# Optimization experiments

Hardware: AMD Instinct MI355X
Metric: run time of the kernel (lower is better)

## Reference

```python
import jax, jax.numpy as jnp
import numpy as np
import math

EMBED_DIM = 1024
NUM_HEADS = 16
HEAD_DIM = EMBED_DIM // NUM_HEADS


def setup_inputs() -> dict:
    key = jax.random.key(0)
    ks = jax.random.split(key, 12)
    B, N = 2, 2048
    s = 1.0 / math.sqrt(EMBED_DIM)
    inp = {
        "query": jax.random.normal(ks[0], (B, N, EMBED_DIM), jnp.float32),
        "key": jax.random.normal(ks[1], (B, N, EMBED_DIM), jnp.float32),
        "value": jax.random.normal(ks[2], (B, N, EMBED_DIM), jnp.float32),
        "Wq": jax.random.normal(ks[3], (EMBED_DIM, EMBED_DIM), jnp.float32) * s,
        "bq": jnp.zeros((EMBED_DIM,), jnp.float32),
        "Wk": jax.random.normal(ks[4], (EMBED_DIM, EMBED_DIM), jnp.float32) * s,
        "bk": jnp.zeros((EMBED_DIM,), jnp.float32),
        "Wv": jax.random.normal(ks[5], (EMBED_DIM, EMBED_DIM), jnp.float32) * s,
        "bv": jnp.zeros((EMBED_DIM,), jnp.float32),
        "Wo": jax.random.normal(ks[6], (EMBED_DIM, EMBED_DIM), jnp.float32) * s,
        "bo": jnp.zeros((EMBED_DIM,), jnp.float32),
        "gate": jnp.zeros((NUM_HEADS,), jnp.float32),
    }
    return inp


def reference(query, key, value, Wq, bq, Wk, bk, Wv, bv, Wo, bo, gate):
    B, Nq, _ = query.shape
    Nk = key.shape[1]
    H, D = NUM_HEADS, HEAD_DIM
    # projections (Linear: x @ W.T + b); split heads -> [B, H, N, D]
    q = (query @ Wq.T + bq).reshape(B, Nq, H, D).transpose(0, 2, 1, 3)
    k = (key @ Wk.T + bk).reshape(B, Nk, H, D).transpose(0, 2, 1, 3)
    v = (value @ Wv.T + bv).reshape(B, Nk, H, D).transpose(0, 2, 1, 3)
    # scaled logits with per-head sigmoid gate folded into the scale
    scale = jax.nn.sigmoid(gate) / math.sqrt(D)  # [H]
    logits = jnp.einsum("bhqd,bhkd->bhqk", q, k) * scale[None, :, None, None]
    attn = jax.nn.softmax(logits, axis=-1)
    out = jnp.einsum("bhqk,bhkd->bhqd", attn, v)
    out = out.transpose(0, 2, 1, 3).reshape(B, Nq, H * D)
    return out @ Wo.T + bo
```

## Files before the change

kernel.cpp:

```cpp
#include <hip/hip_runtime.h>
#include <hip/hip_bf16.h>
#include <cstdint>


#define DEV __device__ __forceinline__
typedef __attribute__((ext_vector_type(8))) short bf16x8;
typedef __attribute__((ext_vector_type(4))) float f32x4;
typedef unsigned short u16;

DEV void async16(const void* g, void* l) {
  __builtin_amdgcn_global_load_lds(
      (const __attribute__((address_space(1))) unsigned int*)g,
      (__attribute__((address_space(3))) unsigned int*)l, 16, 0, 0);
}

DEV u16 bf16_rne(float f) {
  unsigned int u = __builtin_bit_cast(unsigned int, f);
  u += 0x7FFFu + ((u >> 16) & 1u);
  return (u16)(u >> 16);
}

DEV u16 cvt16(float x) {
  __hip_bfloat16 h = __float2bfloat16(x);
  return __builtin_bit_cast(u16, h);
}

DEV unsigned cvtpk(float lo, float hi) {
  unsigned r;
  asm("v_cvt_pk_bf16_f32 %0, %1, %2" : "=v"(r) : "v"(lo), "v"(hi));
  return r;
}

DEV uint4 cvt8(float4 a, float4 b) {
  uint4 v;
  v.x = cvtpk(a.x, a.y);
  v.y = cvtpk(a.z, a.w);
  v.z = cvtpk(b.x, b.y);
  v.w = cvtpk(b.z, b.w);
  return v;
}

__global__ __launch_bounds__(256, 3) void gemm_qkv(
    const float* __restrict__ Xq, const float* __restrict__ Xk, const float* __restrict__ Xv,
    const float* __restrict__ Wqf, const float* __restrict__ Wkf, const float* __restrict__ Wvf,
    const float* __restrict__ bq, const float* __restrict__ bkb, const float* __restrict__ bv,
    const float* __restrict__ gate,
    u16* __restrict__ QB, u16* __restrict__ KB, u16* __restrict__ VTB) {
  __shared__ __attribute__((aligned(16))) u16 As[2][128 * 32];
  __shared__ __attribute__((aligned(16))) u16 Bs[2][128 * 32];
  const int t = threadIdx.x, lane = t & 63, w = t >> 6;
  const int l15 = lane & 15, quad = lane >> 4;
  const int xcd = blockIdx.x & 7, idx = blockIdx.x >> 3;
  const int seg = idx >> 5, r5 = idx & 31;
  const int bm = (xcd << 2) + (r5 >> 3), bn = r5 & 7;
  const int m0 = bm << 7, n0 = bn << 7;
  const float* A = (seg == 0) ? Xq : (seg == 1) ? Xk : Xv;
  const float* W = (seg == 0) ? Wqf : (seg == 1) ? Wkf : Wvf;
  const int wm = (w >> 1) << 6, wn = (w & 1) << 6;
  const int r0 = t >> 2, cc0 = (t & 3) * 8;
  const float* gA0 = A + (long)(m0 + r0) * 1024 + cc0;
  const float* gA1 = gA0 + 64 * 1024;
  const float* gB0 = W + (long)(n0 + r0) * 1024 + cc0;
  const float* gB1 = gB0 + 64 * 1024;

  float4 ra0, ra1, ra2, ra3, rb0, rb1, rb2, rb3;
  auto LOADA = [&](int ko) {
    const float4* p0 = (const float4*)(gA0 + ko);
    const float4* p1 = (const float4*)(gA1 + ko);
    ra0 = p0[0]; ra1 = p0[1]; ra2 = p1[0]; ra3 = p1[1];
  };
  auto LOADB = [&](int ko) {
    const float4* p0 = (const float4*)(gB0 + ko);
    const float4* p1 = (const float4*)(gB1 + ko);
    rb0 = p0[0]; rb1 = p0[1]; rb2 = p1[0]; rb3 = p1[1];
  };
  auto WRITEA = [&](int nb) {
    *(uint4*)&As[nb][t * 8] = cvt8(ra0, ra1);
    *(uint4*)&As[nb][(t + 256) * 8] = cvt8(ra2, ra3);
  };
  auto WRITEB = [&](int nb) {
    *(uint4*)&Bs[nb][t * 8] = cvt8(rb0, rb1);
    *(uint4*)&Bs[nb][(t + 256) * 8] = cvt8(rb2, rb3);
  };

  LOADA(0); LOADB(0);
  WRITEA(0); WRITEB(0);
  LOADA(32); LOADB(32);

  f32x4 acc[4][4] = {};
  for (int k0 = 0; k0 < 1024; k0 += 32) {
    const int cur = (k0 >> 5) & 1;
    __syncthreads();
    if (k0 + 32 < 1024) {
      const int nb = cur ^ 1;
      WRITEA(nb); WRITEB(nb);
      if (k0 + 64 < 1024) { LOADA(k0 + 64); LOADB(k0 + 64); }
    }
    bf16x8 af[4], bfm[4];
#pragma unroll
    for (int i = 0; i < 4; i++)
      af[i] = *(const bf16x8*)&As[cur][(wm + i * 16 + l15) * 32 + quad * 8];
#pragma unroll
    for (int j = 0; j < 4; j++)
      bfm[j] = *(const bf16x8*)&Bs[cur][(wn + j * 16 + l15) * 32 + quad * 8];
#pragma unroll
    for (int i = 0; i < 4; i++)
#pragma unroll
      for (int j = 0; j < 4; j++)
        acc[i][j] = __builtin_amdgcn_mfma_f32_16x16x32_bf16(af[i], bfm[j], acc[i][j], 0, 0, 0);
  }

  if (seg == 2) {
#pragma unroll
    for (int i = 0; i < 4; i++) {
      int token = m0 + wm + i * 16 + quad * 4;
      int bb_ = token >> 11, n = token & 2047;
#pragma unroll
      for (int j = 0; j < 4; j++) {
        int col = n0 + wn + j * 16 + l15;
        float bb = bv[col];
        union { u16 us[4]; uint2 u2; } pk;
#pragma unroll
        for (int r = 0; r < 4; r++) pk.us[r] = bf16_rne(acc[i][j][r] + bb);
        *(uint2*)&VTB[(long)(bb_ * 1024 + col) * 2048 + n] = pk.u2;
      }
    }
  } else {
    const float* bias = seg ? bkb : bq;
    u16* C = seg ? KB : QB;
#pragma unroll
    for (int j = 0; j < 4; j++) {
      int col = n0 + wn + j * 16 + l15;
      float bb = bias[col];
      float scl = 1.f;
      if (seg == 0) {
        float g = gate[col >> 6];
        float sig = 1.f / (1.f + __builtin_amdgcn_exp2f(-g * 1.44269504f));
        scl = sig * 0.125f * 1.44269504f;
      }
#pragma unroll
      for (int i = 0; i < 4; i++) {
        int row = m0 + wm + i * 16 + quad * 4;
#pragma unroll
        for (int r = 0; r < 4; r++)
          C[(long)(row + r) * 1024 + col] = bf16_rne((acc[i][j][r] + bb) * scl);
      }
    }
  }
}

__global__ __launch_bounds__(256, 4) void gemm_out(
    const u16* __restrict__ A, const float* __restrict__ Wof,
    const float* __restrict__ bias, float* __restrict__ Cf) {
  __shared__ __attribute__((aligned(16))) u16 As[2][64 * 32];
  __shared__ __attribute__((aligned(16))) u16 Bs[2][64 * 32];
  const int t = threadIdx.x, lane = t & 63, w = t >> 6;
  const int l15 = lane & 15, quad = lane >> 4;
  const int xcd = blockIdx.x & 7, idx = blockIdx.x >> 3;
  const int bm = (xcd << 3) + (idx >> 4), bn = idx & 15;
  const int m0 = bm << 6, n0 = bn << 6;
  const int wm = (w >> 1) << 5, wn = (w & 1) << 5;
  const int r0 = t >> 2, cc0 = (t & 3) * 8;
  const u16* gA = A + (long)(m0 + r0) * 1024 + cc0;
  const float* gB = Wof + (long)(n0 + r0) * 1024 + cc0;

  float4 rb0, rb1;
  auto LOADB = [&](int ko) {
    const float4* p = (const float4*)(gB + ko);
    rb0 = p[0]; rb1 = p[1];
  };
  auto WRITEB = [&](int nb) {
    *(uint4*)&Bs[nb][t * 8] = cvt8(rb0, rb1);
  };

  async16(gA, &As[0][t * 8]);
  LOADB(0); WRITEB(0); LOADB(32);

  f32x4 acc[2][2] = {};
  for (int k0 = 0; k0 < 1024; k0 += 32) {
    const int cur = (k0 >> 5) & 1;
    __syncthreads();
    if (k0 + 32 < 1024) {
      const int kn = k0 + 32, nb = cur ^ 1;
      async16(gA + kn, &As[nb][t * 8]);
      WRITEB(nb);
      if (k0 + 64 < 1024) LOADB(k0 + 64);
    }
    bf16x8 af[2], bfm[2];
#pragma unroll
    for (int i = 0; i < 2; i++)
      af[i] = *(const bf16x8*)&As[cur][(wm + i * 16 + l15) * 32 + quad * 8];
#pragma unroll
    for (int j = 0; j < 2; j++)
      bfm[j] = *(const bf16x8*)&Bs[cur][(wn + j * 16 + l15) * 32 + quad * 8];
#pragma unroll
    for (int i = 0; i < 2; i++)
#pragma unroll
      for (int j = 0; j < 2; j++)
        acc[i][j] = __builtin_amdgcn_mfma_f32_16x16x32_bf16(af[i], bfm[j], acc[i][j], 0, 0, 0);
  }

#pragma unroll
  for (int j = 0; j < 2; j++) {
    int col = n0 + wn + j * 16 + l15;
    float bb = bias[col];
#pragma unroll
    for (int i = 0; i < 2; i++) {
      int row = m0 + wm + i * 16 + quad * 4;
#pragma unroll
      for (int r = 0; r < 4; r++)
        Cf[(long)(row + r) * 1024 + col] = acc[i][j][r] + bb;
    }
  }
}

__global__ __launch_bounds__(256, 4) void attn_kernel(
    const u16* __restrict__ Q, const u16* __restrict__ Kb,
    const u16* __restrict__ Vt, u16* __restrict__ Op0, u16* __restrict__ Op3,
    float* __restrict__ lp) {
  __shared__ __attribute__((aligned(16))) u16 Ks[2][32 * 64];
  __shared__ __attribute__((aligned(16))) u16 Vs[2][64 * 32];
  const int t = threadIdx.x, lane = t & 63, w = t >> 6;
  const int l15 = lane & 15, quad = lane >> 4;
  const int xcd = blockIdx.x & 7, rr = blockIdx.x >> 3;
  const int ksp = xcd >> 1, qt = ((xcd & 1) << 3) | rr;
  const int h = blockIdx.y, b = blockIdx.z;
  const int q0 = qt * 128, tok0 = b * 2048, key0 = ksp * 512;
  const u16* Kbase = Kb + (long)tok0 * 1024 + h * 64;
  const u16* Vbase = Vt + (long)(b * 1024 + h * 64) * 2048 + key0;

  bf16x8 aq[2][2];
#pragma unroll
  for (int i = 0; i < 2; i++) {
    long row = tok0 + q0 + w * 32 + i * 16 + l15;
#pragma unroll
    for (int ks = 0; ks < 2; ks++)
      aq[i][ks] = *(const bf16x8*)&Q[row * 1024 + h * 64 + ks * 32 + quad * 8];
  }

  const int rk = t >> 3, ck = t & 7;
  const int rv = t >> 2, cv = t & 3;
  const u16* kg = Kbase + (long)(key0 + rk) * 1024 + ((ck ^ ((rk >> 1) & 7)) * 8);
  const u16* vg = Vbase + (long)rv * 2048 + ((cv ^ ((rv >> 1) & 3)) * 8);
  u16* ksd = &Ks[0][t * 8];
  u16* vsd = &Vs[0][t * 8];

  auto STAGE = [&](int tk, int bu) {
    async16(kg + (long)tk * 32768, ksd + bu * 2048);
    async16(vg + tk * 32, vsd + bu * 2048);
  };

  STAGE(0, 0);

  float l_st[2] = {};
  f32x4 O[2][4] = {};

  for (int kt = 0; kt < 16; kt++) {
    const int cur = kt & 1;
    __syncthreads();
    if (kt + 1 < 16) STAGE(kt + 1, cur ^ 1);

    f32x4 s[2][2] = {};
    __builtin_amdgcn_s_setprio(1);
#pragma unroll
    for (int ks = 0; ks < 2; ks++) {
      bf16x8 bk_[2];
#pragma unroll
      for (int j = 0; j < 2; j++) {
        int rl = 2 * l15 + j;
        bk_[j] = *(const bf16x8*)&Ks[cur][rl * 64 + (((ks * 4 + quad) ^ (l15 & 7))) * 8];
      }
#pragma unroll
      for (int i = 0; i < 2; i++)
#pragma unroll
        for (int j = 0; j < 2; j++)
          s[i][j] = __builtin_amdgcn_mfma_f32_16x16x32_bf16(bk_[j], aq[i][ks], s[i][j], 0, 0, 0);
    }
    __builtin_amdgcn_s_setprio(0);

    bf16x8 ap[2];
#pragma unroll
    for (int i = 0; i < 2; i++) {
      union { unsigned uw[4]; bf16x8 v8; } pw;
#pragma unroll
      for (int r = 0; r < 4; r++) {
        float p0 = __builtin_amdgcn_exp2f(s[i][0][r]);
        float p1 = __builtin_amdgcn_exp2f(s[i][1][r]);
        l_st[i] += p0 + p1;
        pw.uw[r] = cvtpk(p0, p1);
      }
      ap[i] = pw.v8;
    }

    bf16x8 bv_[4];
#pragma unroll
    for (int dj = 0; dj < 4; dj++) {
      int rl = dj * 16 + l15;
      bv_[dj] = *(const bf16x8*)&Vs[cur][rl * 32 + ((quad ^ ((rl >> 1) & 3))) * 8];
    }
    __builtin_amdgcn_s_setprio(1);
#pragma unroll
    for (int i = 0; i < 2; i++)
#pragma unroll
      for (int dj = 0; dj < 4; dj++)
        O[i][dj] = __builtin_amdgcn_mfma_f32_16x16x32_bf16(ap[i], bv_[dj], O[i][dj], 0, 0, 0);
    __builtin_amdgcn_s_setprio(0);
  }

  u16* dst = (ksp == 3) ? Op3 : (Op0 + (long)ksp * 4194304);
#pragma unroll
  for (int i = 0; i < 2; i++) {
    float ls = l_st[i];
    ls += __shfl_xor(ls, 16); ls += __shfl_xor(ls, 32);
    if (quad == 0) {
      long qrow = tok0 + q0 + w * 32 + i * 16 + l15;
      lp[ksp * 65536 + (int)qrow * 16 + h] = ls;
    }
#pragma unroll
    for (int r = 0; r < 4; r++) {
      long row = tok0 + q0 + w * 32 + i * 16 + quad * 4 + r;
#pragma unroll
      for (int dj = 0; dj < 4; dj++)
        dst[row * 1024 + h * 64 + dj * 16 + l15] = cvt16(O[i][dj][r]);
    }
  }
}

__global__ __launch_bounds__(256) void merge_kernel(
    const u16* __restrict__ Op0, const u16* __restrict__ Op3,
    const float* __restrict__ lp, u16* __restrict__ AO) {
  int idx = blockIdx.x * 256 + threadIdx.x;
  int tok = idx >> 7, rem = idx & 127, h = rem >> 3;
  int li = tok * 16 + h;
  float inv = 1.f / (lp[li] + lp[65536 + li] + lp[131072 + li] + lp[196608 + li]);
  union U { uint4 v; u16 us[8]; };
  U a0, a1, a2, a3, uo;
  a0.v = ((const uint4*)Op0)[idx];
  a1.v = ((const uint4*)Op0)[idx + 524288];
  a2.v = ((const uint4*)Op0)[idx + 1048576];
  a3.v = ((const uint4*)Op3)[idx];
#pragma unroll
  for (int j = 0; j < 8; j++) {
    float f0 = __builtin_bit_cast(float, (unsigned)((unsigned)a0.us[j] << 16));
    float f1 = __builtin_bit_cast(float, (unsigned)((unsigned)a1.us[j] << 16));
    float f2 = __builtin_bit_cast(float, (unsigned)((unsigned)a2.us[j] << 16));
    float f3 = __builtin_bit_cast(float, (unsigned)((unsigned)a3.us[j] << 16));
    uo.us[j] = cvt16((f0 + f1 + f2 + f3) * inv);
  }
  ((uint4*)AO)[idx] = uo.v;
}

extern "C" void kernel_launch(void* const* d_in, const int* in_sizes, int n_in,
                              void* d_out, int out_size, void* d_ws, size_t ws_size,
                              hipStream_t stream) {
  const float* q  = (const float*)d_in[0];
  const float* k  = (const float*)d_in[1];
  const float* v  = (const float*)d_in[2];
  const float* Wq = (const float*)d_in[3];
  const float* bq = (const float*)d_in[4];
  const float* Wk = (const float*)d_in[5];
  const float* bk = (const float*)d_in[6];
  const float* Wv = (const float*)d_in[7];
  const float* bv = (const float*)d_in[8];
  const float* Wo = (const float*)d_in[9];
  const float* bo = (const float*)d_in[10];
  const float* gate = (const float*)d_in[11];
  float* out = (float*)d_out;
  char* ws = (char*)d_ws;

  const size_t MB = 1u << 20;
  u16* QB  = (u16*)(ws + 32 * MB);
  u16* KB  = (u16*)(ws + 40 * MB);
  u16* OPp  = (u16*)(ws + 8 * MB);
  u16* OPd3 = (u16*)((char*)d_out + 8 * MB);
  float* LP = (float*)(ws + 0 * MB);
  u16* AOB  = (u16*)(ws + 8 * MB);
  u16* VTB  = (u16*)d_out;

  gemm_qkv<<<768, 256, 0, stream>>>(q, k, v, Wq, Wk, Wv, bq, bk, bv, gate,
                                    QB, KB, VTB);
  attn_kernel<<<dim3(64, 16, 2), 256, 0, stream>>>(QB, KB, VTB, OPp, OPd3, LP);
  merge_kernel<<<2048, 256, 0, stream>>>(OPp, OPd3, LP, AOB);
  gemm_out<<<1024, 256, 0, stream>>>(AOB, Wo, bo, out);
}
```

Before: 230.5 us.

## Pre-cast QKV weights to bf16, halve key splits, fuse merge into output GEMM

Adds a pre-pass that casts Wq/Wk/Wv to bf16 so the QKV GEMM can stream the B operand straight into LDS with async loads instead of converting fp32 in registers. Attention now uses 2 key splits of 1024 keys instead of 4 of 512, launching half as many blocks, each doing twice as many key tiles. The separate merge kernel is removed: the output GEMM reads the two partial outputs and the row sums, combines and normalizes them while staging its A tile. This saves a launch and a full pass over intermediate data, at the cost of less attention parallelism, an extra cast kernel, and register-path loads in the output GEMM.

```diff
diff --git a/kernel.cpp b/kernel.cpp
--- a/kernel.cpp
+++ b/kernel.cpp
@@ -40,9 +40,25 @@
   return v;
 }
 
+DEV float bfu(u16 u) {
+  return __builtin_bit_cast(float, (unsigned)((unsigned)u << 16));
+}
+
+__global__ __launch_bounds__(256) void cast_w(
+    const float* __restrict__ Wq, const float* __restrict__ Wk,
+    const float* __restrict__ Wv, u16* __restrict__ WB) {
+  int idx = blockIdx.x * 256 + threadIdx.x;
+  const float* src; int i;
+  if      (idx < 131072) { src = Wq; i = idx; }
+  else if (idx < 262144) { src = Wk; i = idx - 131072; }
+  else                   { src = Wv; i = idx - 262144; }
+  const float4* p = (const float4*)src + (size_t)i * 2;
+  ((uint4*)WB)[idx] = cvt8(p[0], p[1]);
+}
+
 __global__ __launch_bounds__(256, 3) void gemm_qkv(
     const float* __restrict__ Xq, const float* __restrict__ Xk, const float* __restrict__ Xv,
-    const float* __restrict__ Wqf, const float* __restrict__ Wkf, const float* __restrict__ Wvf,
+    const u16* __restrict__ Wb,
     const float* __restrict__ bq, const float* __restrict__ bkb, const float* __restrict__ bv,
     const float* __restrict__ gate,
     u16* __restrict__ QB, u16* __restrict__ KB, u16* __restrict__ VTB) {
@@ -55,46 +71,39 @@
   const int bm = (xcd << 2) + (r5 >> 3), bn = r5 & 7;
   const int m0 = bm << 7, n0 = bn << 7;
   const float* A = (seg == 0) ? Xq : (seg == 1) ? Xk : Xv;
-  const float* W = (seg == 0) ? Wqf : (seg == 1) ? Wkf : Wvf;
+  const u16* W = Wb + (long)seg * 1048576;
   const int wm = (w >> 1) << 6, wn = (w & 1) << 6;
   const int r0 = t >> 2, cc0 = (t & 3) * 8;
   const float* gA0 = A + (long)(m0 + r0) * 1024 + cc0;
   const float* gA1 = gA0 + 64 * 1024;
-  const float* gB0 = W + (long)(n0 + r0) * 1024 + cc0;
-  const float* gB1 = gB0 + 64 * 1024;
-
-  float4 ra0, ra1, ra2, ra3, rb0, rb1, rb2, rb3;
+  const u16* gB0 = W + (long)(n0 + r0) * 1024 + cc0;
+  const u16* gB1 = gB0 + 64 * 1024;
+
+  float4 ra0, ra1, ra2, ra3;
   auto LOADA = [&](int ko) {
     const float4* p0 = (const float4*)(gA0 + ko);
     const float4* p1 = (const float4*)(gA1 + ko);
     ra0 = p0[0]; ra1 = p0[1]; ra2 = p1[0]; ra3 = p1[1];
   };
-  auto LOADB = [&](int ko) {
-    const float4* p0 = (const float4*)(gB0 + ko);
-    const float4* p1 = (const float4*)(gB1 + ko);
-    rb0 = p0[0]; rb1 = p0[1]; rb2 = p1[0]; rb3 = p1[1];
-  };
   auto WRITEA = [&](int nb) {
     *(uint4*)&As[nb][t * 8] = cvt8(ra0, ra1);
     *(uint4*)&As[nb][(t + 256) * 8] = cvt8(ra2, ra3);
   };
-  auto WRITEB = [&](int nb) {
-    *(uint4*)&Bs[nb][t * 8] = cvt8(rb0, rb1);
-    *(uint4*)&Bs[nb][(t + 256) * 8] = cvt8(rb2, rb3);
-  };
-
-  LOADA(0); LOADB(0);
-  WRITEA(0); WRITEB(0);
-  LOADA(32); LOADB(32);
+
+  LOADA(0);
+  async16(gB0, &Bs[0][t * 8]); async16(gB1, &Bs[0][(t + 256) * 8]);
+  WRITEA(0);
+  LOADA(32);
 
   f32x4 acc[4][4] = {};
   for (int k0 = 0; k0 < 1024; k0 += 32) {
     const int cur = (k0 >> 5) & 1;
     __syncthreads();
     if (k0 + 32 < 1024) {
-      const int nb = cur ^ 1;
-      WRITEA(nb); WRITEB(nb);
-      if (k0 + 64 < 1024) { LOADA(k0 + 64); LOADB(k0 + 64); }
+      const int kn = k0 + 32, nb = cur ^ 1;
+      WRITEA(nb);
+      async16(gB0 + kn, &Bs[nb][t * 8]); async16(gB1 + kn, &Bs[nb][(t + 256) * 8]);
+      if (k0 + 64 < 1024) LOADA(k0 + 64);
     }
     bf16x8 af[4], bfm[4];
 #pragma unroll
@@ -150,8 +159,9 @@
 }
 
 __global__ __launch_bounds__(256, 4) void gemm_out(
-    const u16* __restrict__ A, const float* __restrict__ Wof,
-    const float* __restrict__ bias, float* __restrict__ Cf) {
+    const u16* __restrict__ Op0, const float* __restrict__ lp,
+    const float* __restrict__ Wof, const float* __restrict__ bias,
+    float* __restrict__ Cf) {
   __shared__ __attribute__((aligned(16))) u16 As[2][64 * 32];
   __shared__ __attribute__((aligned(16))) u16 Bs[2][64 * 32];
   const int t = threadIdx.x, lane = t & 63, w = t >> 6;
@@ -161,10 +171,28 @@
   const int m0 = bm << 6, n0 = bn << 6;
   const int wm = (w >> 1) << 5, wn = (w & 1) << 5;
   const int r0 = t >> 2, cc0 = (t & 3) * 8;
-  const u16* gA = A + (long)(m0 + r0) * 1024 + cc0;
+  const uint4* gA0u = (const uint4*)Op0 + (((long)(m0 + r0) * 1024 + cc0) >> 3);
   const float* gB = Wof + (long)(n0 + r0) * 1024 + cc0;
 
+  uint4 au0, au1; float ainv;
   float4 rb0, rb1;
+  auto LOADA = [&](int ko) {
+    au0 = gA0u[ko >> 3];
+    au1 = gA0u[524288 + (ko >> 3)];
+    int li = (m0 + r0) * 16 + (ko >> 6);
+    ainv = 1.f / (lp[li] + lp[65536 + li]);
+  };
+  auto WRITEA = [&](int nb) {
+    const u16* p0 = (const u16*)&au0;
+    const u16* p1 = (const u16*)&au1;
+    float f[8];
+#pragma unroll
+    for (int j = 0; j < 8; j++) f[j] = (bfu(p0[j]) + bfu(p1[j])) * ainv;
+    uint4 v;
+    v.x = cvtpk(f[0], f[1]); v.y = cvtpk(f[2], f[3]);
+    v.z = cvtpk(f[4], f[5]); v.w = cvtpk(f[6], f[7]);
+    *(uint4*)&As[nb][t * 8] = v;
+  };
   auto LOADB = [&](int ko) {
     const float4* p = (const float4*)(gB + ko);
     rb0 = p[0]; rb1 = p[1];
@@ -173,18 +201,18 @@
     *(uint4*)&Bs[nb][t * 8] = cvt8(rb0, rb1);
   };
 
-  async16(gA, &As[0][t * 8]);
-  LOADB(0); WRITEB(0); LOADB(32);
+  LOADA(0); LOADB(0);
+  WRITEA(0); WRITEB(0);
+  LOADA(32); LOADB(32);
 
   f32x4 acc[2][2] = {};
   for (int k0 = 0; k0 < 1024; k0 += 32) {
     const int cur = (k0 >> 5) & 1;
     __syncthreads();
     if (k0 + 32 < 1024) {
-      const int kn = k0 + 32, nb = cur ^ 1;
-      async16(gA + kn, &As[nb][t * 8]);
-      WRITEB(nb);
-      if (k0 + 64 < 1024) LOADB(k0 + 64);
+      const int nb = cur ^ 1;
+      WRITEA(nb); WRITEB(nb);
+      if (k0 + 64 < 1024) { LOADA(k0 + 64); LOADB(k0 + 64); }
     }
     bf16x8 af[2], bfm[2];
 #pragma unroll
@@ -216,16 +244,15 @@
 
 __global__ __launch_bounds__(256, 4) void attn_kernel(
     const u16* __restrict__ Q, const u16* __restrict__ Kb,
-    const u16* __restrict__ Vt, u16* __restrict__ Op0, u16* __restrict__ Op3,
-    float* __restrict__ lp) {
+    const u16* __restrict__ Vt, u16* __restrict__ Op0, float* __restrict__ lp) {
   __shared__ __attribute__((aligned(16))) u16 Ks[2][32 * 64];
   __shared__ __attribute__((aligned(16))) u16 Vs[2][64 * 32];
   const int t = threadIdx.x, lane = t & 63, w = t >> 6;
   const int l15 = lane & 15, quad = lane >> 4;
   const int xcd = blockIdx.x & 7, rr = blockIdx.x >> 3;
-  const int ksp = xcd >> 1, qt = ((xcd & 1) << 3) | rr;
+  const int ksp = xcd >> 2, qt = ((xcd & 3) << 2) | rr;
   const int h = blockIdx.y, b = blockIdx.z;
-  const int q0 = qt * 128, tok0 = b * 2048, key0 = ksp * 512;
+  const int q0 = qt * 128, tok0 = b * 2048, key0 = ksp * 1024;
   const u16* Kbase = Kb + (long)tok0 * 1024 + h * 64;
   const u16* Vbase = Vt + (long)(b * 1024 + h * 64) * 2048 + key0;
 
@@ -255,10 +282,10 @@
   float l_st[2] = {};
   f32x4 O[2][4] = {};
 
-  for (int kt = 0; kt < 16; kt++) {
+  for (int kt = 0; kt < 32; kt++) {
     const int cur = kt & 1;
     __syncthreads();
-    if (kt + 1 < 16) STAGE(kt + 1, cur ^ 1);
+    if (kt + 1 < 32) STAGE(kt + 1, cur ^ 1);
 
     f32x4 s[2][2] = {};
     __builtin_amdgcn_s_setprio(1);
@@ -307,7 +334,7 @@
     __builtin_amdgcn_s_setprio(0);
   }
 
-  u16* dst = (ksp == 3) ? Op3 : (Op0 + (long)ksp * 4194304);
+  u16* dst = Op0 + (long)ksp * 4194304;
 #pragma unroll
   for (int i = 0; i < 2; i++) {
     float ls = l_st[i];
@@ -324,30 +351,6 @@
         dst[row * 1024 + h * 64 + dj * 16 + l15] = cvt16(O[i][dj][r]);
     }
   }
-}
-
-__global__ __launch_bounds__(256) void merge_kernel(
-    const u16* __restrict__ Op0, const u16* __restrict__ Op3,
-    const float* __restrict__ lp, u16* __restrict__ AO) {
-  int idx = blockIdx.x * 256 + threadIdx.x;
-  int tok = idx >> 7, rem = idx & 127, h = rem >> 3;
-  int li = tok * 16 + h;
-  float inv = 1.f / (lp[li] + lp[65536 + li] + lp[131072 + li] + lp[196608 + li]);
-  union U { uint4 v; u16 us[8]; };
-  U a0, a1, a2, a3, uo;
-  a0.v = ((const uint4*)Op0)[idx];
-  a1.v = ((const uint4*)Op0)[idx + 524288];
-  a2.v = ((const uint4*)Op0)[idx + 1048576];
-  a3.v = ((const uint4*)Op3)[idx];
-#pragma unroll
-  for (int j = 0; j < 8; j++) {
-    float f0 = __builtin_bit_cast(float, (unsigned)((unsigned)a0.us[j] << 16));
-    float f1 = __builtin_bit_cast(float, (unsigned)((unsigned)a1.us[j] << 16));
-    float f2 = __builtin_bit_cast(float, (unsigned)((unsigned)a2.us[j] << 16));
-    float f3 = __builtin_bit_cast(float, (unsigned)((unsigned)a3.us[j] << 16));
-    uo.us[j] = cvt16((f0 + f1 + f2 + f3) * inv);
-  }
-  ((uint4*)AO)[idx] = uo.v;
 }
 
 extern "C" void kernel_launch(void* const* d_in, const int* in_sizes, int n_in,
@@ -369,17 +372,15 @@
   char* ws = (char*)d_ws;
 
   const size_t MB = 1u << 20;
-  u16* QB  = (u16*)(ws + 32 * MB);
-  u16* KB  = (u16*)(ws + 40 * MB);
+  u16* WB   = (u16*)(ws + 0 * MB);
+  u16* QB   = (u16*)(ws + 32 * MB);
+  u16* KB   = (u16*)(ws + 40 * MB);
   u16* OPp  = (u16*)(ws + 8 * MB);
-  u16* OPd3 = (u16*)((char*)d_out + 8 * MB);
   float* LP = (float*)(ws + 0 * MB);
-  u16* AOB  = (u16*)(ws + 8 * MB);
   u16* VTB  = (u16*)d_out;
 
-  gemm_qkv<<<768, 256, 0, stream>>>(q, k, v, Wq, Wk, Wv, bq, bk, bv, gate,
-                                    QB, KB, VTB);
-  attn_kernel<<<dim3(64, 16, 2), 256, 0, stream>>>(QB, KB, VTB, OPp, OPd3, LP);
-  merge_kernel<<<2048, 256, 0, stream>>>(OPp, OPd3, LP, AOB);
-  gemm_out<<<1024, 256, 0, stream>>>(AOB, Wo, bo, out);
-}
+  cast_w<<<1536, 256, 0, stream>>>(Wq, Wk, Wv, WB);
+  gemm_qkv<<<768, 256, 0, stream>>>(q, k, v, WB, bq, bk, bv, gate, QB, KB, VTB);
+  attn_kernel<<<dim3(32, 16, 2), 256, 0, stream>>>(QB, KB, VTB, OPp, LP);
+  gemm_out<<<1024, 256, 0, stream>>>(OPp, LP, Wo, bo, out);
+}
```

Measured after the change: 248.0 us. 1.08x slower.
